# Optimization experiments

Hardware: AMD Instinct MI355X
Metric: run time of the kernel (lower is better)

The kernel has to match this reference:

```python
import jax, jax.numpy as jnp
import numpy as np

BEV_H = 512
BEV_W = 512


def setup_inputs() -> dict:
    key = jax.random.key(0)
    k1, k2, k3, k4 = jax.random.split(key, 4)
    P, C, B = 200000, 64, 4
    pillar_feats = jax.random.normal(k1, (P, C), dtype=jnp.float32)
    b_idx = jax.random.randint(k2, (P,), 0, B, dtype=jnp.int32)
    r_idx = jax.random.randint(k3, (P,), 0, BEV_H, dtype=jnp.int32)
    c_idx = jax.random.randint(k4, (P,), 0, BEV_W, dtype=jnp.int32)
    coords = jnp.stack([b_idx, r_idx, c_idx], axis=1)  # (P, 3) int32
    return {"pillar_feats": pillar_feats, "coords": coords, "batch_size": B}


def reference(pillar_feats, coords, batch_size):
    # pillar_feats: (P, C) float; coords: (P, 3) int (batch, row, col)
    H, W = BEV_H, BEV_W
    P, C = pillar_feats.shape
    b = coords[:, 0].astype(jnp.int32)
    r = jnp.clip(coords[:, 1].astype(jnp.int32), 0, H - 1)
    c = jnp.clip(coords[:, 2].astype(jnp.int32), 0, W - 1)
    flat_key = b * (H * W) + r * W + c  # (P,)
    # index that maps to it (equivalent to the module's dedup + unique scatter).
    last = jnp.full((batch_size * H * W,), -1, dtype=jnp.int32)
    last = last.at[flat_key].max(jnp.arange(P, dtype=jnp.int32))  # (B*H*W,)
    valid = last >= 0
    gathered = pillar_feats[jnp.clip(last, 0)]  # (B*H*W, C)
    bev_flat = jnp.where(valid[:, None], gathered, jnp.zeros((), pillar_feats.dtype))
    bev = bev_flat.reshape(batch_size, H, W, C).transpose(0, 3, 1, 2)  # (B, C, H, W)
    return bev
```

## Files before the change

kernel.cpp:

```cpp
#include <hip/hip_runtime.h>

#define BEV_H 512
#define BEV_W 512
#define CCH   64
#define HW    (BEV_H * BEV_W)
#define CHW   (CCH * HW)

__global__ void bev_fill_neg1(int* __restrict__ out_i, int B) {
    int t = blockIdx.x * blockDim.x + threadIdx.x;
    const int per_b4 = HW / 4;
    if (t >= B * per_b4) return;
    int b  = t / per_b4;
    int i4 = t - b * per_b4;
    int4* p = reinterpret_cast<int4*>(out_i + (size_t)b * CHW);
    p[i4] = make_int4(-1, -1, -1, -1);
}

__global__ void bev_scatter_max(const int* __restrict__ coords,
                                int* __restrict__ out_i, int P) {
    int p = blockIdx.x * blockDim.x + threadIdx.x;
    if (p >= P) return;
    int b = coords[p * 3 + 0];
    int r = coords[p * 3 + 1];
    int c = coords[p * 3 + 2];
    r = min(max(r, 0), BEV_H - 1);
    c = min(max(c, 0), BEV_W - 1);
    size_t key = (size_t)b * CHW + (size_t)r * BEV_W + c;
    atomicMax(&out_i[key], p);
}

__global__ void bev_gather(const float* __restrict__ feats,
                           float* __restrict__ out, int ncell4) {
    int t = blockIdx.x * blockDim.x + threadIdx.x;
    if (t >= ncell4) return;

    const int W4 = BEV_W / 4;
    int c4 = t % W4;
    int br = t / W4;
    int r  = br % BEV_H;
    int b  = br / BEV_H;

    size_t base = (size_t)b * CHW + (size_t)r * BEV_W + (size_t)c4 * 4;
    const int4 l4 = *reinterpret_cast<const int4*>(
        reinterpret_cast<const int*>(out) + base);

    const float* f0 = (l4.x >= 0) ? feats + (size_t)l4.x * CCH : nullptr;
    const float* f1 = (l4.y >= 0) ? feats + (size_t)l4.y * CCH : nullptr;
    const float* f2 = (l4.z >= 0) ? feats + (size_t)l4.z * CCH : nullptr;
    const float* f3 = (l4.w >= 0) ? feats + (size_t)l4.w * CCH : nullptr;

    float* outp = out + base;
    const float4 zero = make_float4(0.f, 0.f, 0.f, 0.f);

#pragma unroll
    for (int g = 0; g < CCH / 4; ++g) {
        float4 a = f0 ? *reinterpret_cast<const float4*>(f0 + g * 4) : zero;
        float4 bb = f1 ? *reinterpret_cast<const float4*>(f1 + g * 4) : zero;
        float4 cc = f2 ? *reinterpret_cast<const float4*>(f2 + g * 4) : zero;
        float4 dd = f3 ? *reinterpret_cast<const float4*>(f3 + g * 4) : zero;

        float4 v0 = make_float4(a.x, bb.x, cc.x, dd.x);
        float4 v1 = make_float4(a.y, bb.y, cc.y, dd.y);
        float4 v2 = make_float4(a.z, bb.z, cc.z, dd.z);
        float4 v3 = make_float4(a.w, bb.w, cc.w, dd.w);

        float* o = outp + (size_t)(g * 4) * HW;
        *reinterpret_cast<float4*>(o)              = v0;
        *reinterpret_cast<float4*>(o + (size_t)HW) = v1;
        *reinterpret_cast<float4*>(o + 2*(size_t)HW) = v2;
        *reinterpret_cast<float4*>(o + 3*(size_t)HW) = v3;
    }
}

extern "C" void kernel_launch(void* const* d_in, const int* in_sizes, int n_in,
                              void* d_out, int out_size, void* d_ws, size_t ws_size,
                              hipStream_t stream) {
    const float* feats  = (const float*)d_in[0];
    const int*   coords = (const int*)d_in[1];

    const int P = in_sizes[0] / CCH;
    const int B = out_size / CHW;
    const int ncell  = B * HW;
    const int ncell4 = ncell / 4;

    float* out  = (float*)d_out;
    int*   outi = (int*)d_out;

    {
        int n = ncell4;
        int threads = 256;
        int blocks = (n + threads - 1) / threads;
        bev_fill_neg1<<<blocks, threads, 0, stream>>>(outi, B);
    }
    {
        int threads = 256;
        int blocks = (P + threads - 1) / threads;
        bev_scatter_max<<<blocks, threads, 0, stream>>>(coords, outi, P);
    }
    {
        int threads = 256;
        int blocks = (ncell4 + threads - 1) / threads;
        bev_gather<<<blocks, threads, 0, stream>>>(feats, out, ncell4);
    }
}
```

Measured before the change: 338.8 us.

## Stage gathered pillar rows in shared memory tile and transpose for channel-plane writes

```diff
diff --git a/kernel.cpp b/kernel.cpp
--- a/kernel.cpp
+++ b/kernel.cpp
@@ -5,6 +5,9 @@
 #define CCH   64
 #define HW    (BEV_H * BEV_W)
 #define CHW   (CCH * HW)
+
+#define CELLS   128
+#define THREADS 256
 
 __global__ void bev_fill_neg1(int* __restrict__ out_i, int B) {
     int t = blockIdx.x * blockDim.x + threadIdx.x;
@@ -29,46 +32,50 @@
     atomicMax(&out_i[key], p);
 }
 
-__global__ void bev_gather(const float* __restrict__ feats,
-                           float* __restrict__ out, int ncell4) {
-    int t = blockIdx.x * blockDim.x + threadIdx.x;
-    if (t >= ncell4) return;
+__global__ __launch_bounds__(THREADS, 4)
+void bev_gather(const float* __restrict__ feats, float* __restrict__ out) {
+    __shared__ float tile[CELLS][CCH + 1];
+    __shared__ int   shwin[CELLS];
 
-    const int W4 = BEV_W / 4;
-    int c4 = t % W4;
-    int br = t / W4;
-    int r  = br % BEV_H;
-    int b  = br / BEV_H;
+    const int t    = threadIdx.x;
+    const int blk  = blockIdx.x;
+    const int cell0 = blk * CELLS;
+    const int c0   = cell0 & (BEV_W - 1);
+    const int br   = cell0 / BEV_W;
+    const int b    = br >> 9;
+    const int r    = br & (BEV_H - 1);
 
-    size_t base = (size_t)b * CHW + (size_t)r * BEV_W + (size_t)c4 * 4;
-    const int4 l4 = *reinterpret_cast<const int4*>(
-        reinterpret_cast<const int*>(out) + base);
+    const int* winplane = reinterpret_cast<const int*>(out)
+                        + (size_t)b * CHW + (size_t)r * BEV_W + c0;
+    if (t < CELLS) shwin[t] = winplane[t];
+    __syncthreads();
 
-    const float* f0 = (l4.x >= 0) ? feats + (size_t)l4.x * CCH : nullptr;
-    const float* f1 = (l4.y >= 0) ? feats + (size_t)l4.y * CCH : nullptr;
-    const float* f2 = (l4.z >= 0) ? feats + (size_t)l4.z * CCH : nullptr;
-    const float* f3 = (l4.w >= 0) ? feats + (size_t)l4.w * CCH : nullptr;
+    const int w     = t >> 6;
+    const int l     = t & 63;
+    const int chunk = l & 15;
+    const int sub   = l >> 4;
+#pragma unroll
+    for (int it = 0; it < CELLS / 16; ++it) {
+        int cell = it * 16 + w * 4 + sub;
+        int win  = shwin[cell];
+        float4 v = make_float4(0.f, 0.f, 0.f, 0.f);
+        if (win >= 0)
+            v = *reinterpret_cast<const float4*>(
+                    feats + (size_t)win * CCH + chunk * 4);
+        *reinterpret_cast<float4*>(&tile[cell][chunk * 4]) = v;
+    }
+    __syncthreads();
 
-    float* outp = out + base;
-    const float4 zero = make_float4(0.f, 0.f, 0.f, 0.f);
-
+    const int ch = t >> 2;
+    const int q  = t & 3;
+    float* chbase = out + (size_t)b * CHW + (size_t)ch * HW
+                  + (size_t)r * BEV_W + c0;
 #pragma unroll
-    for (int g = 0; g < CCH / 4; ++g) {
-        float4 a = f0 ? *reinterpret_cast<const float4*>(f0 + g * 4) : zero;
-        float4 bb = f1 ? *reinterpret_cast<const float4*>(f1 + g * 4) : zero;
-        float4 cc = f2 ? *reinterpret_cast<const float4*>(f2 + g * 4) : zero;
-        float4 dd = f3 ? *reinterpret_cast<const float4*>(f3 + g * 4) : zero;
-
-        float4 v0 = make_float4(a.x, bb.x, cc.x, dd.x);
-        float4 v1 = make_float4(a.y, bb.y, cc.y, dd.y);
-        float4 v2 = make_float4(a.z, bb.z, cc.z, dd.z);
-        float4 v3 = make_float4(a.w, bb.w, cc.w, dd.w);
-
-        float* o = outp + (size_t)(g * 4) * HW;
-        *reinterpret_cast<float4*>(o)              = v0;
-        *reinterpret_cast<float4*>(o + (size_t)HW) = v1;
-        *reinterpret_cast<float4*>(o + 2*(size_t)HW) = v2;
-        *reinterpret_cast<float4*>(o + 3*(size_t)HW) = v3;
+    for (int i = 0; i < 8; ++i) {
+        int cell = i * 16 + q * 4;
+        float4 v = make_float4(tile[cell + 0][ch], tile[cell + 1][ch],
+                               tile[cell + 2][ch], tile[cell + 3][ch]);
+        *reinterpret_cast<float4*>(chbase + cell) = v;
     }
 }
 
@@ -80,26 +87,22 @@
 
     const int P = in_sizes[0] / CCH;
     const int B = out_size / CHW;
-    const int ncell  = B * HW;
-    const int ncell4 = ncell / 4;
+    const int ncell = B * HW;
 
     float* out  = (float*)d_out;
     int*   outi = (int*)d_out;
 
     {
-        int n = ncell4;
-        int threads = 256;
-        int blocks = (n + threads - 1) / threads;
-        bev_fill_neg1<<<blocks, threads, 0, stream>>>(outi, B);
+        int n = ncell / 4;
+        int blocks = (n + 255) / 256;
+        bev_fill_neg1<<<blocks, 256, 0, stream>>>(outi, B);
     }
     {
-        int threads = 256;
-        int blocks = (P + threads - 1) / threads;
-        bev_scatter_max<<<blocks, threads, 0, stream>>>(coords, outi, P);
+        int blocks = (P + 255) / 256;
+        bev_scatter_max<<<blocks, 256, 0, stream>>>(coords, outi, P);
     }
     {
-        int threads = 256;
-        int blocks = (ncell4 + threads - 1) / threads;
-        bev_gather<<<blocks, threads, 0, stream>>>(feats, out, ncell4);
+        int blocks = ncell / CELLS;
+        bev_gather<<<blocks, THREADS, 0, stream>>>(feats, out);
     }
 }
```

Result: slower. 359.3 us (+6.1%).
